# Performance work log

Measured on AMD Instinct MI355X. Metric: run time of the kernel, lower is better.

The kernel has to match this reference:

```python
import jax, jax.numpy as jnp
import numpy as np

B, T, K, H = 8192, 96, 32, 768  # batch, max_len, output_dim (tags), bert hidden


def setup_inputs() -> dict:
    key = jax.random.key(0)
    k1, k2, k3, k4 = jax.random.split(key, 4)
    hidden = jax.random.normal(k1, (B, H), dtype=jnp.float32)
    target = jax.random.randint(k2, (B, T), 0, K, dtype=jnp.int32)
    # Dense(output_dim * max_len) params
    W = jax.random.normal(k3, (H, T * K), dtype=jnp.float32) * 0.02
    b = jnp.zeros((T * K,), dtype=jnp.float32)
    # tf.random.uniform transition matrix
    transitions = jax.random.uniform(k4, (K, K), dtype=jnp.float32)
    return {"hidden": hidden, "target": target, "W": W, "b": b, "transitions": transitions}


def _crf_log_norm(em_tm, transitions):
    # em_tm: [T, B, K] time-major emissions. Forward algorithm (logsumexp recurrence).
    def step(alpha, em_t):
        # alpha: [B, K]; broadcast over next-tag axis
        new = jax.nn.logsumexp(alpha[:, :, None] + transitions[None, :, :], axis=1) + em_t
        return new, None
    alpha, _ = jax.lax.scan(step, em_tm[0], em_tm[1:])
    return jax.nn.logsumexp(alpha, axis=-1)  # [B]


def _crf_sequence_score(em_btk, target, transitions):
    # unary: emission score at gold tags; binary: transition scores along gold path
    unary = jnp.take_along_axis(em_btk, target[..., None], axis=-1)[..., 0].sum(-1)
    binary = transitions[target[:, :-1], target[:, 1:]].sum(-1)
    return unary + binary  # [B]


def _viterbi_decode(em_tm, transitions):
    # em_tm: [T, B, K]. Max-product forward pass collecting backpointers.
    def fwd(v, em_t):
        scores = v[:, :, None] + transitions[None, :, :]  # [B, K_prev, K_next]
        bp = jnp.argmax(scores, axis=1).astype(jnp.int32)  # [B, K]
        return jnp.max(scores, axis=1) + em_t, bp
    v, bps = jax.lax.scan(fwd, em_tm[0], em_tm[1:])  # bps: [T-1, B, K]
    last_tag = jnp.argmax(v, axis=-1).astype(jnp.int32)  # [B]
    # backtrace (reverse scan); output index i is the tag at time i
    def back(tag, bp_t):
        prev = jnp.take_along_axis(bp_t, tag[:, None], axis=1)[:, 0]
        return prev, prev
    _, prevs = jax.lax.scan(back, last_tag, bps, reverse=True)  # [T-1, B]
    tags = jnp.concatenate([prevs, last_tag[None, :]], axis=0)  # [T, B]
    return jnp.transpose(tags), jnp.max(v, axis=-1)


def reference(hidden, target, W, b, transitions):
    # Dense with sigmoid, then reshape to (B, max_len, output_dim)
    em = jax.nn.sigmoid(hidden @ W + b).reshape(hidden.shape[0], T, K)
    em_tm = jnp.transpose(em, (1, 0, 2))  # time-major for scan
    log_likelihood = _crf_sequence_score(em, target, transitions) - _crf_log_norm(em_tm, transitions)
    decode_predict, _ = _viterbi_decode(em_tm, transitions)
    return decode_predict, log_likelihood
```

## Files before the change

### kernel.cpp

```cpp
#include <hip/hip_runtime.h>
#include <cstdint>
#include <cstddef>

#define B_  8192
#define T_  96
#define K_  32
#define H_  768
#define NK_ (T_ * K_)

typedef __attribute__((ext_vector_type(8))) _Float16 f16x8;
typedef __attribute__((ext_vector_type(4))) float    f32x4;

#define SCALE_UP   4096.0f
#define SCALE_DOWN (1.0f / 16777216.0f)

__device__ __forceinline__ void load_lds16(const void* g, void* l) {
    __builtin_amdgcn_global_load_lds(
        (const __attribute__((address_space(1))) unsigned int*)g,
        (__attribute__((address_space(3))) unsigned int*)l,
        16, 0, 0);
}

__global__ __launch_bounds__(256) void splitA_kernel(
    const float* __restrict__ A, _Float16* __restrict__ Ath, _Float16* __restrict__ Atl)
{
    const int g   = blockIdx.x * 256 + threadIdx.x;
    const int row = g / 96;
    const int o   = g - row * 96;
    const int ks  = o >> 2, qq = o & 3;
    const int r   = row & 127, rb = row >> 7;
    const size_t dst = (size_t)(rb * 24 + ks) * 4096 + r * 32 + ((qq ^ ((r >> 1) & 3)) << 3);

    f32x4 v0 = *(const f32x4*)(A + (size_t)row * H_ + o * 8);
    f32x4 v1 = *(const f32x4*)(A + (size_t)row * H_ + o * 8 + 4);
    f16x8 hi, lo;
#pragma unroll
    for (int e = 0; e < 8; e++) {
        float x = ((e < 4) ? v0[e] : v1[e - 4]) * SCALE_UP;
        _Float16 h = (_Float16)x;
        hi[e] = h;
        lo[e] = (_Float16)(x - (float)h);
    }
    *(f16x8*)&Ath[dst] = hi;
    *(f16x8*)&Atl[dst] = lo;
}

__global__ __launch_bounds__(256) void splitW_kernel(
    const float* __restrict__ W, _Float16* __restrict__ Wth, _Float16* __restrict__ Wtl)
{
    const int g   = blockIdx.x * 256 + threadIdx.x;
    const int ko  = g / NK_;
    const int col = g - ko * NK_;
    const int k0  = ko * 8;
    const int cb  = col >> 7, n = col & 127;
    const int ks  = k0 >> 5, qq = (k0 & 31) >> 3;
    const size_t dst = (size_t)(cb * 24 + ks) * 4096 + n * 32 + ((qq ^ ((n >> 1) & 3)) << 3);

    f16x8 hi, lo;
#pragma unroll
    for (int j = 0; j < 8; j++) {
        float x = W[(size_t)(k0 + j) * NK_ + col] * SCALE_UP;
        _Float16 h = (_Float16)x;
        hi[j] = h;
        lo[j] = (_Float16)(x - (float)h);
    }
    *(f16x8*)&Wth[dst] = hi;
    *(f16x8*)&Wtl[dst] = lo;
}

__global__ __launch_bounds__(256, 2) void gemm_mfma_sigmoid_kernel(
    const _Float16* __restrict__ Ath, const _Float16* __restrict__ Atl,
    const _Float16* __restrict__ Wth, const _Float16* __restrict__ Wtl,
    const float* __restrict__ bias, float* __restrict__ em)
{
    __shared__ _Float16 lds[2][4][4096];

    const int tid  = threadIdx.x;
    const int bid  = blockIdx.x;
    const int wgid = (bid & 7) * 192 + (bid >> 3);
    const int cb   = wgid % 24;
    const int rb   = wgid / 24;
    const int lane = tid & 63;
    const int w    = tid >> 6;
    const int wr   = w >> 1, wc = w & 1;
    const int fr   = lane & 15;
    const int kg   = lane >> 4;

    const _Float16* srcs[4] = {
        Ath + (size_t)(rb * 24) * 4096, Atl + (size_t)(rb * 24) * 4096,
        Wth + (size_t)(cb * 24) * 4096, Wtl + (size_t)(cb * 24) * 4096 };

    auto stage = [&](int ks, int bb) {
#pragma unroll
        for (int m = 0; m < 4; m++) {
            const _Float16* s = srcs[m] + (size_t)ks * 4096 + w * 1024 + lane * 8;
            _Float16* d = &lds[bb][m][w * 1024];
            load_lds16(s, d);
            load_lds16(s + 512, d + 512);
        }
    };

    f32x4 acc[4][4];
#pragma unroll
    for (int i = 0; i < 4; i++)
#pragma unroll
        for (int j = 0; j < 4; j++) acc[i][j] = (f32x4)0.0f;

    int cur = 0;
    stage(0, 0);

    for (int ks = 0; ks < 24; ks++) {
        __syncthreads();
        if (ks + 1 < 24) stage(ks + 1, cur ^ 1);

        f16x8 fah[4], fal[4], fbh[4], fbl[4];
#pragma unroll
        for (int mi = 0; mi < 4; mi++) {
            const int r   = wr * 64 + mi * 16 + fr;
            const int idx = r * 32 + ((kg ^ ((r >> 1) & 3)) << 3);
            fah[mi] = *(const f16x8*)&lds[cur][0][idx];
            fal[mi] = *(const f16x8*)&lds[cur][1][idx];
        }
#pragma unroll
        for (int ni = 0; ni < 4; ni++) {
            const int r   = wc * 64 + ni * 16 + fr;
            const int idx = r * 32 + ((kg ^ ((r >> 1) & 3)) << 3);
            fbh[ni] = *(const f16x8*)&lds[cur][2][idx];
            fbl[ni] = *(const f16x8*)&lds[cur][3][idx];
        }
#pragma unroll
        for (int mi = 0; mi < 4; mi++)
#pragma unroll
            for (int ni = 0; ni < 4; ni++) {
                acc[mi][ni] = __builtin_amdgcn_mfma_f32_16x16x32_f16(fah[mi], fbh[ni], acc[mi][ni], 0, 0, 0);
                acc[mi][ni] = __builtin_amdgcn_mfma_f32_16x16x32_f16(fah[mi], fbl[ni], acc[mi][ni], 0, 0, 0);
                acc[mi][ni] = __builtin_amdgcn_mfma_f32_16x16x32_f16(fal[mi], fbh[ni], acc[mi][ni], 0, 0, 0);
            }
        cur ^= 1;
    }

    const int er = rb * 128 + wr * 64 + (lane >> 4) * 4;
    const int ec = cb * 128 + wc * 64 + fr;
#pragma unroll
    for (int ni = 0; ni < 4; ni++) {
        const int   gc = ec + ni * 16;
        const float bv = bias[gc];
#pragma unroll
        for (int mi = 0; mi < 4; mi++)
#pragma unroll
            for (int r = 0; r < 4; r++) {
                const int gr = er + mi * 16 + r;
                float x = acc[mi][ni][r] * SCALE_DOWN + bv;
                em[(size_t)gr * NK_ + gc] = 1.0f / (1.0f + __expf(-x));
            }
    }
}


#define VSTEP(T_, SH_, WI_)                                               \
  {                                                                       \
    const float cem = na; na = emb[((T_) + 1) * K_];                      \
    vxs[k] = va;                                                          \
    __builtin_amdgcn_wave_barrier();                                      \
    float bva = -1e30f; int bia = 0;                                      \
    _Pragma("unroll")                                                     \
    for (int j = 0; j < 8; j++) {                                         \
      f32x4 vq = *(const f32x4*)&vxs[4 * j];                              \
      float s0 = vq[0] + tca[4 * j];                                      \
      float s1 = vq[1] + tca[4 * j + 1];                                  \
      float s2 = vq[2] + tca[4 * j + 2];                                  \
      float s3 = vq[3] + tca[4 * j + 3];                                  \
      float w0 = (s1 > s0) ? s1 : s0;                                     \
      int   i0 = (s1 > s0) ? (4 * j + 1) : (4 * j);                       \
      float w1 = (s3 > s2) ? s3 : s2;                                     \
      int   i1 = (s3 > s2) ? (4 * j + 3) : (4 * j + 2);                   \
      if (w1 > w0) { w0 = w1; i0 = i1; }                                  \
      if (w0 > bva) { bva = w0; bia = i0; }                               \
    }                                                                     \
    va = bva + cem;                                                       \
    bpw |= (unsigned int)bia << (5 * (SH_));                              \
    if ((SH_) == 5) { bps[k * 17 + (WI_)] = bpw; bpw = 0; }               \
    __builtin_amdgcn_wave_barrier();                                      \
  }

__global__ __launch_bounds__(256, 4) void crf_roles_kernel(
    const float* __restrict__ em,
    const int* __restrict__ target,
    const float* __restrict__ trans,
    float* __restrict__ out_tags,
    float* __restrict__ ll)
{
    __shared__ float trans_s[K_ * K_];
    __shared__ float Eex[4][36];
    __shared__ float vex[4][36];
    __shared__ unsigned int bp5[4][545];
    __shared__ unsigned char tgt_s[4][T_];

    const int tid  = threadIdx.x;
    const int w    = tid >> 6;
    const int lane = tid & 63;
    const int half = lane >> 5;
    const int k    = lane & 31;
    const bool isFwd = (w < 2);
    const int s    = (((isFwd ? w : w - 2) << 1) | half);
    const int b    = blockIdx.x * 4 + s;

    for (int i = tid; i < K_ * K_; i += 256) trans_s[i] = trans[i];
    __syncthreads();

    const float* emb = em + (size_t)b * NK_ + k;

    if (isFwd) {
        float Ea2[K_];
#pragma unroll
        for (int p = 0; p < K_; p++) Ea2[p] = __expf(trans_s[p * K_ + k]);

        const int t0 = target[b * T_ + k];
        const int t1 = target[b * T_ + 32 + k];
        const int t2 = target[b * T_ + 64 + k];
        tgt_s[s][k]      = (unsigned char)t0;
        tgt_s[s][k + 32] = (unsigned char)t1;
        tgt_s[s][k + 64] = (unsigned char)t2;
        __builtin_amdgcn_wave_barrier();
        const float* emrow = em + (size_t)b * NK_;
        float gold = emrow[k * K_ + t0] + emrow[(k + 32) * K_ + t1] + emrow[(k + 64) * K_ + t2];
        if (k > 0) gold += trans_s[(int)tgt_s[s][k - 1] * K_ + t0];
        gold += trans_s[(int)tgt_s[s][k + 31] * K_ + t1];
        gold += trans_s[(int)tgt_s[s][k + 63] * K_ + t2];

        float Ea = __expf(emb[0]);
        int   expo_sum = 0;
        float na = emb[K_];
        float* exs = &Eex[s][0];

        for (int t = 1; t <= 95; ++t) {
            const float cem = na;
            na = emb[(t + 1) * K_];
            exs[k] = Ea;
            __builtin_amdgcn_wave_barrier();
            float fa = 0.0f;
#pragma unroll
            for (int j = 0; j < 8; j++) {
                f32x4 q = *(const f32x4*)&exs[4 * j];
                fa = fmaf(q[0], Ea2[4 * j],     fa);
                fa = fmaf(q[1], Ea2[4 * j + 1], fa);
                fa = fmaf(q[2], Ea2[4 * j + 2], fa);
                fa = fmaf(q[3], Ea2[4 * j + 3], fa);
            }
            Ea = fa * __expf(cem - 4.0f);
            __builtin_amdgcn_wave_barrier();

            if ((t % 12) == 0) {
                float m = Ea;
#pragma unroll
                for (int d = 16; d >= 1; d >>= 1) m = fmaxf(m, __shfl_xor(m, d));
                const unsigned int ebits = (__float_as_uint(m) >> 23) & 255u;
                const float sc = __uint_as_float((254u - ebits) << 23);
                Ea *= sc;
                expo_sum += (int)ebits - 127;
            }
        }

        float S = Ea;
#pragma unroll
        for (int d = 16; d >= 1; d >>= 1) S += __shfl_xor(S, d);
        const float logZ = __logf(S) + 380.0f + (float)expo_sum * 0.69314718055994531f;

        float gs = gold;
#pragma unroll
        for (int d = 16; d >= 1; d >>= 1) gs += __shfl_xor(gs, d);

        if (k == 0) ll[b] = gs - logZ;

    } else {
        float tca[K_];
#pragma unroll
        for (int p = 0; p < K_; p++) tca[p] = trans_s[p * K_ + k];

        float va = emb[0];
        float na = emb[K_];
        unsigned int bpw = 0;
        float* vxs = &vex[s][0];
        unsigned int* bps = &bp5[s][0];

        for (int it = 0; it < 7; ++it) {
            const int tb = it * 12 + 1;
            const int wi = it * 2;
            VSTEP(tb + 0, 0, wi)  VSTEP(tb + 1, 1, wi)  VSTEP(tb + 2, 2, wi)
            VSTEP(tb + 3, 3, wi)  VSTEP(tb + 4, 4, wi)  VSTEP(tb + 5, 5, wi)
            VSTEP(tb + 6, 0, wi + 1)  VSTEP(tb + 7, 1, wi + 1)  VSTEP(tb + 8, 2, wi + 1)
            VSTEP(tb + 9, 3, wi + 1)  VSTEP(tb + 10, 4, wi + 1) VSTEP(tb + 11, 5, wi + 1)
        }
        VSTEP(85, 0, 14) VSTEP(86, 1, 14) VSTEP(87, 2, 14)
        VSTEP(88, 3, 14) VSTEP(89, 4, 14) VSTEP(90, 5, 14)
        VSTEP(91, 0, 15) VSTEP(92, 1, 15) VSTEP(93, 2, 15)
        VSTEP(94, 3, 15) VSTEP(95, 4, 15)
        bps[k * 17 + 15] = bpw;
        __builtin_amdgcn_wave_barrier();

        float bv = va; int bi = k;
#pragma unroll
        for (int d = 16; d >= 1; d >>= 1) {
            float ov = __shfl_xor(bv, d);
            int   oi = __shfl_xor(bi, d);
            if (ov > bv || (ov == bv && oi < bi)) { bv = ov; bi = oi; }
        }

        if (k == 0) {
            float* ot = out_tags + (size_t)b * T_;
            int tag = bi;
            ot[T_ - 1] = (float)tag;
            for (int t = T_ - 2; t >= 0; t--) {
                unsigned int wd = bps[tag * 17 + t / 6];
                tag = (int)((wd >> (5 * (t % 6))) & 31u);
                ot[t] = (float)tag;
            }
        }
    }
}

extern "C" void kernel_launch(void* const* d_in, const int* in_sizes, int n_in,
                              void* d_out, int out_size, void* d_ws, size_t ws_size,
                              hipStream_t stream)
{
    const float* hidden = (const float*)d_in[0];
    const int*   target = (const int*)d_in[1];
    const float* W      = (const float*)d_in[2];
    const float* bias   = (const float*)d_in[3];
    const float* trans  = (const float*)d_in[4];

    float* out      = (float*)d_out;
    float* out_tags = out;
    float* out_ll   = out + (size_t)B_ * T_;

    char* ws = (char*)d_ws;
    const size_t emB = (size_t)B_ * NK_ * 4;
    const size_t ahB = (size_t)B_ * H_ * 2;
    const size_t whB = (size_t)H_ * NK_ * 2;

    float*    em  = (float*)ws;
    _Float16* Ath = (_Float16*)(ws + emB);
    _Float16* Atl = (_Float16*)(ws + emB + ahB);
    _Float16* Wth = (_Float16*)(ws + emB + 2 * ahB);
    _Float16* Wtl = (_Float16*)(ws + emB + 2 * ahB + whB);

    splitA_kernel<<<(B_ * 96) / 256, 256, 0, stream>>>(hidden, Ath, Atl);
    splitW_kernel<<<(NK_ * 96) / 256, 256, 0, stream>>>(W, Wth, Wtl);

    gemm_mfma_sigmoid_kernel<<<1536, 256, 0, stream>>>(Ath, Atl, Wth, Wtl, bias, em);

    crf_roles_kernel<<<B_ / 4, 256, 0, stream>>>(em, target, trans, out_tags, out_ll);
}
```

Before: 250.5 us.

## Store Viterbi score history instead of backpointers and recompute argmax in backtrace

The forward Viterbi loop now keeps only a running max, with no argmax index tracking or packed 5-bit backpointer words. Each step's score vector goes into a per-sequence LDS history buffer. The backtrace recomputes each argmax by a 32-lane shuffle reduction over history plus transitions, with lowest-index tie-breaking. This trims ALU work in the serial forward recurrence, but adds a 95-step shuffle-reduction backtrace and much more LDS (about 48KB per block), which may reduce occupancy below the 4 blocks per CU requested by the launch bounds.

```diff
diff --git a/kernel.cpp b/kernel.cpp
--- a/kernel.cpp
+++ b/kernel.cpp
@@ -156,33 +156,6 @@
     }
 }
 
-
-#define VSTEP(T_, SH_, WI_)                                               \
-  {                                                                       \
-    const float cem = na; na = emb[((T_) + 1) * K_];                      \
-    vxs[k] = va;                                                          \
-    __builtin_amdgcn_wave_barrier();                                      \
-    float bva = -1e30f; int bia = 0;                                      \
-    _Pragma("unroll")                                                     \
-    for (int j = 0; j < 8; j++) {                                         \
-      f32x4 vq = *(const f32x4*)&vxs[4 * j];                              \
-      float s0 = vq[0] + tca[4 * j];                                      \
-      float s1 = vq[1] + tca[4 * j + 1];                                  \
-      float s2 = vq[2] + tca[4 * j + 2];                                  \
-      float s3 = vq[3] + tca[4 * j + 3];                                  \
-      float w0 = (s1 > s0) ? s1 : s0;                                     \
-      int   i0 = (s1 > s0) ? (4 * j + 1) : (4 * j);                       \
-      float w1 = (s3 > s2) ? s3 : s2;                                     \
-      int   i1 = (s3 > s2) ? (4 * j + 3) : (4 * j + 2);                   \
-      if (w1 > w0) { w0 = w1; i0 = i1; }                                  \
-      if (w0 > bva) { bva = w0; bia = i0; }                               \
-    }                                                                     \
-    va = bva + cem;                                                       \
-    bpw |= (unsigned int)bia << (5 * (SH_));                              \
-    if ((SH_) == 5) { bps[k * 17 + (WI_)] = bpw; bpw = 0; }               \
-    __builtin_amdgcn_wave_barrier();                                      \
-  }
-
 __global__ __launch_bounds__(256, 4) void crf_roles_kernel(
     const float* __restrict__ em,
     const int* __restrict__ target,
@@ -191,9 +164,8 @@
     float* __restrict__ ll)
 {
     __shared__ float trans_s[K_ * K_];
-    __shared__ float Eex[4][36];
-    __shared__ float vex[4][36];
-    __shared__ unsigned int bp5[4][545];
+    __shared__ __align__(16) float Eex[4][36];
+    __shared__ __align__(16) float vhist[4][95][K_];
     __shared__ unsigned char tgt_s[4][T_];
 
     const int tid  = threadIdx.x;
@@ -279,24 +251,27 @@
 
         float va = emb[0];
         float na = emb[K_];
-        unsigned int bpw = 0;
-        float* vxs = &vex[s][0];
-        unsigned int* bps = &bp5[s][0];
-
-        for (int it = 0; it < 7; ++it) {
-            const int tb = it * 12 + 1;
-            const int wi = it * 2;
-            VSTEP(tb + 0, 0, wi)  VSTEP(tb + 1, 1, wi)  VSTEP(tb + 2, 2, wi)
-            VSTEP(tb + 3, 3, wi)  VSTEP(tb + 4, 4, wi)  VSTEP(tb + 5, 5, wi)
-            VSTEP(tb + 6, 0, wi + 1)  VSTEP(tb + 7, 1, wi + 1)  VSTEP(tb + 8, 2, wi + 1)
-            VSTEP(tb + 9, 3, wi + 1)  VSTEP(tb + 10, 4, wi + 1) VSTEP(tb + 11, 5, wi + 1)
-        }
-        VSTEP(85, 0, 14) VSTEP(86, 1, 14) VSTEP(87, 2, 14)
-        VSTEP(88, 3, 14) VSTEP(89, 4, 14) VSTEP(90, 5, 14)
-        VSTEP(91, 0, 15) VSTEP(92, 1, 15) VSTEP(93, 2, 15)
-        VSTEP(94, 3, 15) VSTEP(95, 4, 15)
-        bps[k * 17 + 15] = bpw;
-        __builtin_amdgcn_wave_barrier();
+        float* vh = &vhist[s][0][0];
+
+        for (int t = 1; t <= 95; ++t) {
+            const float cem = na;
+            na = emb[(t + 1) * K_];
+            float* row = vh + (t - 1) * K_;
+            row[k] = va;
+            __builtin_amdgcn_wave_barrier();
+            float m = -1e30f;
+#pragma unroll
+            for (int j = 0; j < 8; j++) {
+                f32x4 vq = *(const f32x4*)&row[4 * j];
+                float s0 = vq[0] + tca[4 * j];
+                float s1 = vq[1] + tca[4 * j + 1];
+                float s2 = vq[2] + tca[4 * j + 2];
+                float s3 = vq[3] + tca[4 * j + 3];
+                m = fmaxf(m, fmaxf(fmaxf(s0, s1), fmaxf(s2, s3)));
+            }
+            va = m + cem;
+            __builtin_amdgcn_wave_barrier();
+        }
 
         float bv = va; int bi = k;
 #pragma unroll
@@ -305,16 +280,20 @@
             int   oi = __shfl_xor(bi, d);
             if (ov > bv || (ov == bv && oi < bi)) { bv = ov; bi = oi; }
         }
-
-        if (k == 0) {
-            float* ot = out_tags + (size_t)b * T_;
-            int tag = bi;
-            ot[T_ - 1] = (float)tag;
-            for (int t = T_ - 2; t >= 0; t--) {
-                unsigned int wd = bps[tag * 17 + t / 6];
-                tag = (int)((wd >> (5 * (t % 6))) & 31u);
-                ot[t] = (float)tag;
-            }
+        int tag = bi;
+        if (k == 0) out_tags[(size_t)b * T_ + (T_ - 1)] = (float)tag;
+
+        for (int t = T_ - 2; t >= 0; t--) {
+            float cand = vh[t * K_ + k] + trans_s[k * K_ + tag];
+            float cv = cand; int ci = k;
+#pragma unroll
+            for (int d = 16; d >= 1; d >>= 1) {
+                float ov = __shfl_xor(cv, d);
+                int   oi = __shfl_xor(ci, d);
+                if (ov > cv || (ov == cv && oi < ci)) { cv = ov; ci = oi; }
+            }
+            tag = ci;
+            if (k == 0) out_tags[(size_t)b * T_ + t] = (float)tag;
         }
     }
 }
```

Measured after the change: 378.3 us. 1.51x slower.
